# Performance work log

Measured on AMD Instinct MI355X. Metric: run time of the kernel, lower is better.

## Reference

```python
import jax, jax.numpy as jnp
import numpy as np

B, V, H = 8, 256, 128


def setup_inputs() -> dict:
    key = jax.random.key(0)
    ks = jax.random.split(key, 10)
    s = 0.02
    return {
        "h": jax.random.normal(ks[0], (B, V, H), dtype=jnp.float32),
        "e": jax.random.normal(ks[1], (B, V, V, H), dtype=jnp.float32),
        "graph": jax.random.randint(ks[2], (B, V, V), 0, 2, dtype=jnp.int32),
        "W_pre": jax.random.normal(ks[3], (H, H), dtype=jnp.float32) * s,
        "b_pre": jnp.zeros((H,), dtype=jnp.float32),
        "W_post": jax.random.normal(ks[4], (2 * H, H), dtype=jnp.float32) * s,
        "b_post": jnp.zeros((H,), dtype=jnp.float32),
        "W_skip": jax.random.normal(ks[5], (H, H), dtype=jnp.float32) * s,
        "b_skip": jnp.zeros((H,), dtype=jnp.float32),
    }


def reference(h, e, graph, W_pre, b_pre, W_post, b_post, W_skip, b_skip):
    silu = jax.nn.silu
    # pre self-interaction: (B,V,H)
    h0 = silu(h @ W_pre + b_pre)
    # conv: broadcast multiply edge features by sender node features
    # m[b,i,j,:] = e[b,i,j,:] * h0[b,j,:]
    m = e * h0[:, None, :, :]
    # masked_fill: graph==1 means NO edge -> zero out
    mask = (graph != 0)[..., None]  # (B,V,V,1)
    m = jnp.where(mask, jnp.float32(0), m)
    # max aggregation over neighbors j (dim 2), zeros included as in torch
    neigh = jnp.max(m, axis=2)  # (B,V,H)
    # concat + post self-interaction
    h_cat = jnp.concatenate([h0, neigh], axis=-1)  # (B,V,2H)
    h1 = silu(h_cat @ W_post + b_post)
    # skip interaction + final nonlinearity
    return silu(silu(h @ W_skip + b_skip) + h1)
```

## Files before the change

kernel.cpp:

```cpp
#include <hip/hip_runtime.h>
#include <math.h>

#define BV 2048
#define V_ 256
#define H_ 128

__device__ __forceinline__ float silu_f(float x) {
    return x / (1.0f + expf(-x));
}

__global__ __launch_bounds__(256) void k1_pre_skip(
    const float* __restrict__ h,
    const float* __restrict__ W_pre, const float* __restrict__ b_pre,
    const float* __restrict__ W_skip, const float* __restrict__ b_skip,
    float* __restrict__ h0ws, float* __restrict__ skipws)
{
    const int t = threadIdx.x;
    const int rbase = blockIdx.x * 8;
    __shared__ float s_h[8 * H_];
    #pragma unroll
    for (int q = 0; q < 4; ++q) {
        int flat = q * 256 + t;
        s_h[flat] = h[rbase * H_ + flat];
    }
    __syncthreads();

    const int c  = t & 127;
    const int r0 = (t >> 7) * 4;
    float a0[4] = {0.f, 0.f, 0.f, 0.f};
    float a1[4] = {0.f, 0.f, 0.f, 0.f};
    #pragma unroll 4
    for (int k = 0; k < H_; ++k) {
        float w0 = W_pre[k * H_ + c];
        float w1 = W_skip[k * H_ + c];
        #pragma unroll
        for (int r = 0; r < 4; ++r) {
            float hv = s_h[(r0 + r) * H_ + k];
            a0[r] += hv * w0;
            a1[r] += hv * w1;
        }
    }
    const float bp = b_pre[c], bs = b_skip[c];
    #pragma unroll
    for (int r = 0; r < 4; ++r) {
        int row = rbase + r0 + r;
        h0ws[row * H_ + c]   = silu_f(a0[r] + bp);
        skipws[row * H_ + c] = silu_f(a1[r] + bs);
    }
}

__global__ __launch_bounds__(256, 4) void k2_edge_max(
    const float4* __restrict__ e4,
    const int* __restrict__ graph,
    const float4* __restrict__ h04,
    float* __restrict__ nws)
{
    const int t  = threadIdx.x;
    const int bi = blockIdx.x;
    const int b  = bi >> 8;

    __shared__ int   s_list[V_];
    __shared__ int   s_listT[V_];
    __shared__ int   s_wcnt[4];
    __shared__ float s_red[8 * H_];

    const int  g    = graph[bi * V_ + t];
    const bool keep = (g == 0);
    unsigned long long bal = __ballot(keep);
    const int lane = t & 63;
    const int wv   = t >> 6;
    if (lane == 0) s_wcnt[wv] = __popcll(bal);
    __syncthreads();
    const int count = s_wcnt[0] + s_wcnt[1] + s_wcnt[2] + s_wcnt[3];
    int off = 0;
    for (int w = 0; w < wv; ++w) off += s_wcnt[w];
    if (keep) s_list[off + __popcll(bal & ((1ull << lane) - 1ull))] = t;
    __syncthreads();

    const int j0  = (count > 0) ? s_list[0] : 0;
    {
        const int jgT = t >> 5;
        const int itT = t & 31;
        const int idx = itT * 8 + jgT;
        s_listT[jgT * 32 + itT] = (idx < count) ? s_list[idx] : j0;
    }
    __syncthreads();

    const int h4 = t & 31;
    const int jg = t >> 5;
    const float4* __restrict__ ep = e4 + (size_t)bi * (V_ * 32) + h4;
    const float4* __restrict__ hp = h04 + ((size_t)(b << 8) * 32) + h4;
    const int4*   __restrict__ lt = reinterpret_cast<const int4*>(s_listT) + jg * 8;

    const int chunks = (count + 31) >> 5;
    float4 vmax = make_float4(-INFINITY, -INFINITY, -INFINITY, -INFINITY);
    #pragma unroll 2
    for (int c0 = 0; c0 < chunks; ++c0) {
        int4 j4 = lt[c0];
        float4 ea = ep[j4.x * 32];
        float4 eb = ep[j4.y * 32];
        float4 ec = ep[j4.z * 32];
        float4 ed = ep[j4.w * 32];
        float4 ha = hp[j4.x * 32];
        float4 hb = hp[j4.y * 32];
        float4 hc = hp[j4.z * 32];
        float4 hd = hp[j4.w * 32];
        vmax.x = fmaxf(vmax.x, ea.x * ha.x); vmax.y = fmaxf(vmax.y, ea.y * ha.y);
        vmax.z = fmaxf(vmax.z, ea.z * ha.z); vmax.w = fmaxf(vmax.w, ea.w * ha.w);
        vmax.x = fmaxf(vmax.x, eb.x * hb.x); vmax.y = fmaxf(vmax.y, eb.y * hb.y);
        vmax.z = fmaxf(vmax.z, eb.z * hb.z); vmax.w = fmaxf(vmax.w, eb.w * hb.w);
        vmax.x = fmaxf(vmax.x, ec.x * hc.x); vmax.y = fmaxf(vmax.y, ec.y * hc.y);
        vmax.z = fmaxf(vmax.z, ec.z * hc.z); vmax.w = fmaxf(vmax.w, ec.w * hc.w);
        vmax.x = fmaxf(vmax.x, ed.x * hd.x); vmax.y = fmaxf(vmax.y, ed.y * hd.y);
        vmax.z = fmaxf(vmax.z, ed.z * hd.z); vmax.w = fmaxf(vmax.w, ed.w * hd.w);
    }

    *reinterpret_cast<float4*>(&s_red[jg * H_ + h4 * 4]) = vmax;
    __syncthreads();
    if (t < H_) {
        float m = s_red[t];
        #pragma unroll
        for (int gg = 1; gg < 8; ++gg) m = fmaxf(m, s_red[gg * H_ + t]);
        if (count < V_) m = fmaxf(m, 0.0f);
        nws[bi * H_ + t] = m;
    }
}

__global__ __launch_bounds__(256) void k3_post(
    const float* __restrict__ h0ws,
    const float* __restrict__ nws,
    const float* __restrict__ skipws,
    const float* __restrict__ W_post, const float* __restrict__ b_post,
    float* __restrict__ out)
{
    const int t = threadIdx.x;
    const int rbase = blockIdx.x * 8;
    __shared__ float s_cat[8 * 256];
    #pragma unroll
    for (int q = 0; q < 8; ++q) {
        int flat = q * 256 + t;
        int row  = flat >> 8;
        int k    = flat & 255;
        float v  = (k < H_) ? h0ws[(rbase + row) * H_ + k]
                            : nws[(rbase + row) * H_ + (k - H_)];
        s_cat[flat] = v;
    }
    __syncthreads();

    const int c  = t & 127;
    const int r0 = (t >> 7) * 4;
    float acc[4] = {0.f, 0.f, 0.f, 0.f};
    #pragma unroll 4
    for (int k = 0; k < 256; ++k) {
        float w = W_post[k * H_ + c];
        #pragma unroll
        for (int r = 0; r < 4; ++r)
            acc[r] += s_cat[(r0 + r) * 256 + k] * w;
    }
    const float bp = b_post[c];
    #pragma unroll
    for (int r = 0; r < 4; ++r) {
        int row = rbase + r0 + r;
        float h1 = silu_f(acc[r] + bp);
        out[row * H_ + c] = silu_f(skipws[row * H_ + c] + h1);
    }
}

extern "C" void kernel_launch(void* const* d_in, const int* in_sizes, int n_in,
                              void* d_out, int out_size, void* d_ws, size_t ws_size,
                              hipStream_t stream)
{
    const float* h      = (const float*)d_in[0];
    const float* e      = (const float*)d_in[1];
    const int*   graph  = (const int*)  d_in[2];
    const float* W_pre  = (const float*)d_in[3];
    const float* b_pre  = (const float*)d_in[4];
    const float* W_post = (const float*)d_in[5];
    const float* b_post = (const float*)d_in[6];
    const float* W_skip = (const float*)d_in[7];
    const float* b_skip = (const float*)d_in[8];
    float* out = (float*)d_out;

    float* ws     = (float*)d_ws;
    float* h0ws   = ws;
    float* skipws = ws + BV * H_;
    float* nws    = ws + 2 * BV * H_;

    k1_pre_skip<<<BV / 8, 256, 0, stream>>>(h, W_pre, b_pre, W_skip, b_skip,
                                            h0ws, skipws);
    k2_edge_max<<<BV, 256, 0, stream>>>((const float4*)e, graph,
                                        (const float4*)h0ws, nws);
    k3_post<<<BV / 8, 256, 0, stream>>>(h0ws, nws, skipws, W_post, b_post, out);
}
```

Measured before the change: 392.2 us.

## Fuse post projection into edge-max kernel and widen pre/skip kernel blocks

The post self-interaction matmul now runs inside the edge-max kernel, so each block computes its row's neighbour max, concatenates it with h0 in shared memory and does the W_post GEMV split across two thread halves. This removes the third kernel launch and the round trip of the neighbour tensor through global memory. In exchange each of the 2048 blocks re-reads W_post (128 KB, likely served from L2) instead of amortising it over 8 rows. The pre/skip kernel also moves to 512 threads with 2 rows per thread and vectorised loads.

```diff
diff --git a/kernel.cpp b/kernel.cpp
--- a/kernel.cpp
+++ b/kernel.cpp
@@ -9,7 +9,7 @@
     return x / (1.0f + expf(-x));
 }
 
-__global__ __launch_bounds__(256) void k1_pre_skip(
+__global__ __launch_bounds__(512) void k1_pre_skip(
     const float* __restrict__ h,
     const float* __restrict__ W_pre, const float* __restrict__ b_pre,
     const float* __restrict__ W_skip, const float* __restrict__ b_skip,
@@ -18,23 +18,22 @@
     const int t = threadIdx.x;
     const int rbase = blockIdx.x * 8;
     __shared__ float s_h[8 * H_];
-    #pragma unroll
-    for (int q = 0; q < 4; ++q) {
-        int flat = q * 256 + t;
-        s_h[flat] = h[rbase * H_ + flat];
+    if (t < 256) {
+        reinterpret_cast<float4*>(s_h)[t] =
+            reinterpret_cast<const float4*>(h + (size_t)rbase * H_)[t];
     }
     __syncthreads();
 
     const int c  = t & 127;
-    const int r0 = (t >> 7) * 4;
-    float a0[4] = {0.f, 0.f, 0.f, 0.f};
-    float a1[4] = {0.f, 0.f, 0.f, 0.f};
-    #pragma unroll 4
+    const int r0 = (t >> 7) * 2;
+    float a0[2] = {0.f, 0.f};
+    float a1[2] = {0.f, 0.f};
+    #pragma unroll 8
     for (int k = 0; k < H_; ++k) {
         float w0 = W_pre[k * H_ + c];
         float w1 = W_skip[k * H_ + c];
         #pragma unroll
-        for (int r = 0; r < 4; ++r) {
+        for (int r = 0; r < 2; ++r) {
             float hv = s_h[(r0 + r) * H_ + k];
             a0[r] += hv * w0;
             a1[r] += hv * w1;
@@ -42,18 +41,21 @@
     }
     const float bp = b_pre[c], bs = b_skip[c];
     #pragma unroll
-    for (int r = 0; r < 4; ++r) {
+    for (int r = 0; r < 2; ++r) {
         int row = rbase + r0 + r;
         h0ws[row * H_ + c]   = silu_f(a0[r] + bp);
         skipws[row * H_ + c] = silu_f(a1[r] + bs);
     }
 }
 
-__global__ __launch_bounds__(256, 4) void k2_edge_max(
+__global__ __launch_bounds__(256, 4) void k2_edge_max_post(
     const float4* __restrict__ e4,
     const int* __restrict__ graph,
     const float4* __restrict__ h04,
-    float* __restrict__ nws)
+    const float* __restrict__ h0ws,
+    const float* __restrict__ skipws,
+    const float* __restrict__ W_post, const float* __restrict__ b_post,
+    float* __restrict__ out)
 {
     const int t  = threadIdx.x;
     const int bi = blockIdx.x;
@@ -63,6 +65,8 @@
     __shared__ int   s_listT[V_];
     __shared__ int   s_wcnt[4];
     __shared__ float s_red[8 * H_];
+    __shared__ float s_x[2 * H_];
+    __shared__ float s_part[2 * H_];
 
     const int  g    = graph[bi * V_ + t];
     const bool keep = (g == 0);
@@ -84,6 +88,7 @@
         const int idx = itT * 8 + jgT;
         s_listT[jgT * 32 + itT] = (idx < count) ? s_list[idx] : j0;
     }
+    if (t < H_) s_x[t] = h0ws[bi * H_ + t];
     __syncthreads();
 
     const int h4 = t & 31;
@@ -122,47 +127,23 @@
         #pragma unroll
         for (int gg = 1; gg < 8; ++gg) m = fmaxf(m, s_red[gg * H_ + t]);
         if (count < V_) m = fmaxf(m, 0.0f);
-        nws[bi * H_ + t] = m;
-    }
-}
-
-__global__ __launch_bounds__(256) void k3_post(
-    const float* __restrict__ h0ws,
-    const float* __restrict__ nws,
-    const float* __restrict__ skipws,
-    const float* __restrict__ W_post, const float* __restrict__ b_post,
-    float* __restrict__ out)
-{
-    const int t = threadIdx.x;
-    const int rbase = blockIdx.x * 8;
-    __shared__ float s_cat[8 * 256];
-    #pragma unroll
-    for (int q = 0; q < 8; ++q) {
-        int flat = q * 256 + t;
-        int row  = flat >> 8;
-        int k    = flat & 255;
-        float v  = (k < H_) ? h0ws[(rbase + row) * H_ + k]
-                            : nws[(rbase + row) * H_ + (k - H_)];
-        s_cat[flat] = v;
+        s_x[H_ + t] = m;
     }
     __syncthreads();
 
-    const int c  = t & 127;
-    const int r0 = (t >> 7) * 4;
-    float acc[4] = {0.f, 0.f, 0.f, 0.f};
-    #pragma unroll 4
-    for (int k = 0; k < 256; ++k) {
-        float w = W_post[k * H_ + c];
-        #pragma unroll
-        for (int r = 0; r < 4; ++r)
-            acc[r] += s_cat[(r0 + r) * 256 + k] * w;
+    const int c    = t & 127;
+    const int half = t >> 7;
+    const float* __restrict__ wp = W_post + (size_t)(half * H_) * H_ + c;
+    float acc = 0.f;
+    #pragma unroll 8
+    for (int kk = 0; kk < H_; ++kk) {
+        acc += s_x[half * H_ + kk] * wp[(size_t)kk * H_];
     }
-    const float bp = b_post[c];
-    #pragma unroll
-    for (int r = 0; r < 4; ++r) {
-        int row = rbase + r0 + r;
-        float h1 = silu_f(acc[r] + bp);
-        out[row * H_ + c] = silu_f(skipws[row * H_ + c] + h1);
+    s_part[half * H_ + c] = acc;
+    __syncthreads();
+    if (t < H_) {
+        float h1 = silu_f(s_part[t] + s_part[H_ + t] + b_post[t]);
+        out[bi * H_ + t] = silu_f(skipws[bi * H_ + t] + h1);
     }
 }
 
@@ -184,11 +165,11 @@
     float* ws     = (float*)d_ws;
     float* h0ws   = ws;
     float* skipws = ws + BV * H_;
-    float* nws    = ws + 2 * BV * H_;
 
-    k1_pre_skip<<<BV / 8, 256, 0, stream>>>(h, W_pre, b_pre, W_skip, b_skip,
+    k1_pre_skip<<<BV / 8, 512, 0, stream>>>(h, W_pre, b_pre, W_skip, b_skip,
                                             h0ws, skipws);
-    k2_edge_max<<<BV, 256, 0, stream>>>((const float4*)e, graph,
-                                        (const float4*)h0ws, nws);
-    k3_post<<<BV / 8, 256, 0, stream>>>(h0ws, nws, skipws, W_post, b_post, out);
+    k2_edge_max_post<<<BV, 256, 0, stream>>>((const float4*)e, graph,
+                                             (const float4*)h0ws,
+                                             h0ws, skipws,
+                                             W_post, b_post, out);
 }
```

Result: faster. 365.1 us (-6.9%).
